# Kernel tuning notes

Hardware: AMD Instinct MI355X
Metric: run time of the kernel (lower is better)

Reference implementation:

```python
import jax, jax.numpy as jnp
import numpy as np

B, D = 65536, 1024
E = 10   # experts per group (shared and per-task)
H = 10   # expert hidden units
T = 2    # tasks
G = 20   # gate units = task experts + shared experts


def setup_inputs() -> dict:
    key = jax.random.key(0)
    ks = jax.random.split(key, 8)
    s = 1.0 / np.sqrt(D)
    return {
        "x": jax.random.normal(ks[0], (B, D), dtype=jnp.float32),
        "show_index": jax.random.randint(ks[1], (B,), 0, 100, dtype=jnp.int64),
        "st": jax.random.normal(ks[2], (B, 8), dtype=jnp.float32),
        "Ws": jax.random.normal(ks[3], (E, D, H), dtype=jnp.float32) * s,
        "bs": jnp.zeros((E, H), dtype=jnp.float32),
        "Wt": jax.random.normal(ks[4], (T, E, D, H), dtype=jnp.float32) * s,
        "bt": jnp.zeros((T, E, H), dtype=jnp.float32),
        "Wg": jax.random.normal(ks[5], (T, D, G), dtype=jnp.float32) * s,
        "bg": jnp.zeros((T, G), dtype=jnp.float32),
        "Wc": jax.random.normal(ks[6], (H, 1), dtype=jnp.float32),
        "bc": jnp.zeros((1,), dtype=jnp.float32),
        "Wv": jax.random.normal(ks[7], (H, 1), dtype=jnp.float32),
        "bv": jnp.zeros((1,), dtype=jnp.float32),
    }


def reference(x, show_index, st, Ws, bs, Wt, bt, Wg, bg, Wc, bc, Wv, bv):
    # shared experts: [B, H, E]  (Dense(H,relu) per expert, stacked on axis 2)
    share = jax.nn.relu(jnp.einsum('bd,edh->bhe', x, Ws) + bs.T)

    def task_tower(i):
        gate = jax.nn.softmax(x @ Wg[i] + bg[i], axis=-1)               # [B, G]
        task = jax.nn.relu(jnp.einsum('bd,edh->bhe', x, Wt[i]) + bt[i].T)  # [B, H, E]
        merge = jnp.concatenate([task, share], axis=2)                  # [B, H, G]
        # gate broadcast over H (repeat_elements on axis 1), sum over experts
        return jnp.sum(merge * gate[:, None, :], axis=2)                # [B, H]

    f0 = task_tower(0)
    f1 = task_tower(1)
    ctr_logits = jax.nn.sigmoid(f0 @ Wc + bc)  # [B, 1]
    cvr_logits = jax.nn.sigmoid(f1 @ Wv + bv)  # [B, 1]
    return (ctr_logits, cvr_logits)
```

## Files before the change

### kernel.cpp

```cpp
#include <hip/hip_runtime.h>
#include <hip/hip_bf16.h>

typedef __attribute__((ext_vector_type(8))) short bf16x8;
typedef __attribute__((ext_vector_type(4))) float f32x4;

#define NCOLP 384
#define STEP_SHORTS (NCOLP * 32)
#define STEP_BYTES 24576
#define SEG_BYTES 6144
#define NSTEP 32
#define HSTEP 16
#define BROWS 65536

static __device__ __forceinline__ unsigned int bf16rne(float f) {
  unsigned int u = __float_as_uint(f);
  return (u + 0x7FFFu + ((u >> 16) & 1u)) >> 16;
}
static __device__ __forceinline__ unsigned int pack2(float a, float b) {
  return bf16rne(a) | (bf16rne(b) << 16);
}

__global__ void ple_prep(const float* __restrict__ Ws, const float* __restrict__ bs,
                         const float* __restrict__ Wt, const float* __restrict__ bt,
                         const float* __restrict__ Wg, const float* __restrict__ bg,
                         unsigned short* __restrict__ Wpack, float* __restrict__ bias) {
  const int n = blockIdx.x;
  const int tid = threadIdx.x;
  const float* src = nullptr;
  int stride = 0;
  float bval = 0.f;
  if (n < 200) {
    int t = n / 100, m = n % 100, e = m / 10, h = m % 10;
    src = Wt + (size_t)(t * 10 + e) * 10240 + h;
    stride = 10;
    bval = bt[(t * 10 + e) * 10 + h];
  } else if (n < 300) {
    int m = n - 200, e = m / 10, h = m % 10;
    src = Ws + (size_t)e * 10240 + h;
    stride = 10;
    bval = bs[e * 10 + h];
  } else if (n < 340) {
    int m = n - 300, t = m / 20, g = m % 20;
    src = Wg + (size_t)t * 20480 + g;
    stride = 20;
    bval = bg[t * 20 + g];
  }
  for (int j = 0; j < 4; j++) {
    int k = tid + j * 256;
    float v = src ? src[(size_t)k * stride] : 0.f;
    Wpack[(size_t)(k >> 5) * STEP_SHORTS + ((k >> 3) & 3) * (NCOLP * 8) + n * 8 +
          (k & 7)] = (unsigned short)bf16rne(v);
  }
  if (tid == 0 && n < 352) bias[n] = bval;
}

__global__ __launch_bounds__(256, 2) void ple_main(
    const float* __restrict__ x, const unsigned short* __restrict__ Wpack,
    const float* __restrict__ bias, const float* __restrict__ Wc,
    const float* __restrict__ bc, const float* __restrict__ Wv,
    const float* __restrict__ bv, float* __restrict__ out) {
  __shared__ __align__(16) char smem[65536];
  float* z = (float*)smem;

  const int tid = threadIdx.x;
  const int l = tid & 63, w = tid >> 6;
  const int arow = l & 15, ablk = l >> 4;
  const int rowbase = blockIdx.x * 64;

  const f32x4 fzero = {0.f, 0.f, 0.f, 0.f};
  f32x4 acc[4][6];
#pragma unroll
  for (int i = 0; i < 4; ++i)
#pragma unroll
    for (int j = 0; j < 6; ++j) acc[i][j] = fzero;

  const char* bbase = (const char*)Wpack + ablk * SEG_BYTES +
                      (w * 96 + arow) * 16;
  bf16x8 bA[6], bB[6];

#pragma unroll
  for (int nt = 0; nt < 6; nt++)
    bA[nt] = *(const bf16x8*)(bbase + nt * 256);

  for (int half = 0; half < 2; ++half) {
    {
      const char* xb = (const char*)x + (size_t)(rowbase + w) * 4096 +
                       (size_t)half * 2048 + l * 32;
#pragma unroll 4
      for (int j = 0; j < 16; j++) {
        const float4 f0 = *(const float4*)(xb + (size_t)j * 4 * 4096);
        const float4 f1 = *(const float4*)(xb + (size_t)j * 4 * 4096 + 16);
        const int row = w + j * 4;
        char* dst = smem + row * 1024 + ((l ^ (row & 7)) * 16);
        *(uint4*)dst = make_uint4(pack2(f0.x, f0.y), pack2(f0.z, f0.w),
                                  pack2(f1.x, f1.y), pack2(f1.z, f1.w));
      }
    }
    __syncthreads();

#define STEP(ksl, bc_, bn_)                                                    \
  {                                                                            \
    const int kk = half * HSTEP + (ksl);                                       \
    const int kn = (kk + 1 < NSTEP) ? kk + 1 : NSTEP - 1;                      \
    const char* bp = bbase + (size_t)kn * STEP_BYTES;                          \
    _Pragma("unroll") for (int nt = 0; nt < 6; nt++)                           \
        bn_[nt] = *(const bf16x8*)(bp + nt * 256);                             \
    _Pragma("unroll") for (int mf = 0; mf < 4; mf++) {                         \
      const bf16x8 av = *(const bf16x8*)(smem + (mf * 16 + arow) * 1024 +      \
                                         ((((ksl)*4 + ablk) ^ (arow & 7)) *    \
                                          16));                                \
      _Pragma("unroll") for (int nt = 0; nt < 6; nt++)                         \
          acc[mf][nt] = __builtin_amdgcn_mfma_f32_16x16x32_bf16(               \
              av, bc_[nt], acc[mf][nt], 0, 0, 0);                              \
    }                                                                          \
  }
#pragma unroll
    for (int kp = 0; kp < 8; kp++) {
      STEP(2 * kp, bA, bB)
      STEP(2 * kp + 1, bB, bA)
    }
#undef STEP
    __syncthreads();
  }

#pragma unroll
  for (int p = 0; p < 2; p++) {
    __syncthreads();
#pragma unroll
    for (int q = 0; q < 2; q++) {
      const int mf = p * 2 + q;
#pragma unroll
      for (int nt = 0; nt < 6; nt++) {
        if (w == 3 && nt >= 4) continue;
#pragma unroll
        for (int r = 0; r < 4; r++)
          z[(q * 16 + ablk * 4 + r) * 357 + w * 96 + nt * 16 + arow] =
              acc[mf][nt][r];
      }
    }
    __syncthreads();
    if (tid < 64) {
      const int t = tid >> 5, r = tid & 31;
      const float* zr = &z[r * 357];
      float gl[20], m = -1e30f;
#pragma unroll
      for (int u = 0; u < 20; u++) {
        gl[u] = zr[300 + t * 20 + u] + bias[300 + t * 20 + u];
        m = fmaxf(m, gl[u]);
      }
      float pr[20], s = 0.f;
#pragma unroll
      for (int u = 0; u < 20; u++) {
        pr[u] = __expf(gl[u] - m);
        s += pr[u];
      }
      const float inv = 1.f / s;
      const float* Wl = t ? Wv : Wc;
      float wl[10];
#pragma unroll
      for (int h = 0; h < 10; h++) wl[h] = Wl[h];
      float accum = 0.f;
#pragma unroll
      for (int u = 0; u < 10; u++) {
        float d = 0.f;
#pragma unroll
        for (int h = 0; h < 10; h++) {
          int c = t * 100 + u * 10 + h;
          d += fmaxf(zr[c] + bias[c], 0.f) * wl[h];
        }
        accum += pr[u] * d;
      }
#pragma unroll
      for (int u = 0; u < 10; u++) {
        float d = 0.f;
#pragma unroll
        for (int h = 0; h < 10; h++) {
          int c = 200 + u * 10 + h;
          d += fmaxf(zr[c] + bias[c], 0.f) * wl[h];
        }
        accum += pr[10 + u] * d;
      }
      float logit = (t ? bv[0] : bc[0]) + accum * inv;
      out[(size_t)t * BROWS + rowbase + p * 32 + r] =
          1.f / (1.f + __expf(-logit));
    }
  }
}

extern "C" void kernel_launch(void* const* d_in, const int* in_sizes, int n_in,
                              void* d_out, int out_size, void* d_ws, size_t ws_size,
                              hipStream_t stream) {
  const float* x = (const float*)d_in[0];
  const float* Ws = (const float*)d_in[3];
  const float* bs = (const float*)d_in[4];
  const float* Wt = (const float*)d_in[5];
  const float* bt = (const float*)d_in[6];
  const float* Wg = (const float*)d_in[7];
  const float* bg = (const float*)d_in[8];
  const float* Wc = (const float*)d_in[9];
  const float* bc = (const float*)d_in[10];
  const float* Wv = (const float*)d_in[11];
  const float* bv = (const float*)d_in[12];
  unsigned short* Wpack = (unsigned short*)d_ws;
  float* bias = (float*)((char*)d_ws + (size_t)NCOLP * 1024 * 2);
  float* out = (float*)d_out;

  hipLaunchKernelGGL(ple_prep, dim3(NCOLP), dim3(256), 0, stream, Ws, bs, Wt, bt,
                     Wg, bg, Wpack, bias);
  hipLaunchKernelGGL(ple_main, dim3(BROWS / 64), dim3(256), 0, stream, x, Wpack,
                     bias, Wc, bc, Wv, bv, out);
}
```

Measured before the change: 88.56 us.

## Use 8 waves per block with 48-column slices and quarter-K LDS staging

Doubles the block to 512 threads (8 waves), so each wave computes 48 instead of 96 output columns. This halves the accumulator and B-fragment registers per thread. The x tile is staged in four 256-column quarters in a 32KB LDS buffer instead of two halves in 64KB, with a new swizzle and a load pattern that issues all loads before packing. The aim is higher occupancy and more memory parallelism for the x stream, at the cost of more barriers, more redundant B-weight loads per block, and an epilogue that runs on only 32 threads per 16-row chunk.

```diff
diff --git a/kernel.cpp b/kernel.cpp
--- a/kernel.cpp
+++ b/kernel.cpp
@@ -9,7 +9,6 @@
 #define STEP_BYTES 24576
 #define SEG_BYTES 6144
 #define NSTEP 32
-#define HSTEP 16
 #define BROWS 65536
 
 static __device__ __forceinline__ unsigned int bf16rne(float f) {
@@ -54,12 +53,12 @@
   if (tid == 0 && n < 352) bias[n] = bval;
 }
 
-__global__ __launch_bounds__(256, 2) void ple_main(
+__global__ __launch_bounds__(512, 4) void ple_main(
     const float* __restrict__ x, const unsigned short* __restrict__ Wpack,
     const float* __restrict__ bias, const float* __restrict__ Wc,
     const float* __restrict__ bc, const float* __restrict__ Wv,
     const float* __restrict__ bv, float* __restrict__ out) {
-  __shared__ __align__(16) char smem[65536];
+  __shared__ __align__(16) char smem[32768];
   float* z = (float*)smem;
 
   const int tid = threadIdx.x;
@@ -68,54 +67,63 @@
   const int rowbase = blockIdx.x * 64;
 
   const f32x4 fzero = {0.f, 0.f, 0.f, 0.f};
-  f32x4 acc[4][6];
+  f32x4 acc[4][3];
 #pragma unroll
   for (int i = 0; i < 4; ++i)
 #pragma unroll
-    for (int j = 0; j < 6; ++j) acc[i][j] = fzero;
+    for (int j = 0; j < 3; ++j) acc[i][j] = fzero;
 
   const char* bbase = (const char*)Wpack + ablk * SEG_BYTES +
-                      (w * 96 + arow) * 16;
-  bf16x8 bA[6], bB[6];
-
-#pragma unroll
-  for (int nt = 0; nt < 6; nt++)
+                      (w * 48 + arow) * 16;
+  bf16x8 bA[3], bB[3];
+
+#pragma unroll
+  for (int nt = 0; nt < 3; nt++)
     bA[nt] = *(const bf16x8*)(bbase + nt * 256);
 
-  for (int half = 0; half < 2; ++half) {
+  const int r0 = tid >> 5, s0 = tid & 31;
+  const char* xrow = (const char*)x + (size_t)(rowbase + r0) * 4096 + s0 * 32;
+
+  for (int q = 0; q < 4; ++q) {
     {
-      const char* xb = (const char*)x + (size_t)(rowbase + w) * 4096 +
-                       (size_t)half * 2048 + l * 32;
-#pragma unroll 4
-      for (int j = 0; j < 16; j++) {
-        const float4 f0 = *(const float4*)(xb + (size_t)j * 4 * 4096);
-        const float4 f1 = *(const float4*)(xb + (size_t)j * 4 * 4096 + 16);
-        const int row = w + j * 4;
-        char* dst = smem + row * 1024 + ((l ^ (row & 7)) * 16);
-        *(uint4*)dst = make_uint4(pack2(f0.x, f0.y), pack2(f0.z, f0.w),
-                                  pack2(f1.x, f1.y), pack2(f1.z, f1.w));
+      const char* sbase = xrow + q * 1024;
+      float4 f[8];
+#pragma unroll
+      for (int j = 0; j < 4; j++) {
+        f[2 * j] = *(const float4*)(sbase + (size_t)j * 16 * 4096);
+        f[2 * j + 1] = *(const float4*)(sbase + (size_t)j * 16 * 4096 + 16);
+      }
+#pragma unroll
+      for (int j = 0; j < 4; j++) {
+        const int row = r0 + j * 16;
+        const int segp = (s0 & 24) | ((s0 & 7) ^ (row & 7));
+        *(uint4*)(smem + row * 512 + segp * 16) =
+            make_uint4(pack2(f[2 * j].x, f[2 * j].y),
+                       pack2(f[2 * j].z, f[2 * j].w),
+                       pack2(f[2 * j + 1].x, f[2 * j + 1].y),
+                       pack2(f[2 * j + 1].z, f[2 * j + 1].w));
       }
     }
     __syncthreads();
 
 #define STEP(ksl, bc_, bn_)                                                    \
   {                                                                            \
-    const int kk = half * HSTEP + (ksl);                                       \
+    const int kk = q * 8 + (ksl);                                              \
     const int kn = (kk + 1 < NSTEP) ? kk + 1 : NSTEP - 1;                      \
     const char* bp = bbase + (size_t)kn * STEP_BYTES;                          \
-    _Pragma("unroll") for (int nt = 0; nt < 6; nt++)                           \
+    _Pragma("unroll") for (int nt = 0; nt < 3; nt++)                           \
         bn_[nt] = *(const bf16x8*)(bp + nt * 256);                             \
     _Pragma("unroll") for (int mf = 0; mf < 4; mf++) {                         \
-      const bf16x8 av = *(const bf16x8*)(smem + (mf * 16 + arow) * 1024 +      \
-                                         ((((ksl)*4 + ablk) ^ (arow & 7)) *    \
-                                          16));                                \
-      _Pragma("unroll") for (int nt = 0; nt < 6; nt++)                         \
+      const int segp = ((ksl)*4 & 24) | ((((ksl)&1) * 4 + ablk) ^ (arow & 7)); \
+      const bf16x8 av =                                                        \
+          *(const bf16x8*)(smem + (mf * 16 + arow) * 512 + segp * 16);         \
+      _Pragma("unroll") for (int nt = 0; nt < 3; nt++)                         \
           acc[mf][nt] = __builtin_amdgcn_mfma_f32_16x16x32_bf16(               \
               av, bc_[nt], acc[mf][nt], 0, 0, 0);                              \
     }                                                                          \
   }
 #pragma unroll
-    for (int kp = 0; kp < 8; kp++) {
+    for (int kp = 0; kp < 4; kp++) {
       STEP(2 * kp, bA, bB)
       STEP(2 * kp + 1, bB, bA)
     }
@@ -124,23 +132,18 @@
   }
 
 #pragma unroll
-  for (int p = 0; p < 2; p++) {
-    __syncthreads();
-#pragma unroll
-    for (int q = 0; q < 2; q++) {
-      const int mf = p * 2 + q;
-#pragma unroll
-      for (int nt = 0; nt < 6; nt++) {
-        if (w == 3 && nt >= 4) continue;
+  for (int p = 0; p < 4; p++) {
+#pragma unroll
+    for (int nt = 0; nt < 3; nt++) {
+      if (!(w == 7 && nt >= 1)) {
 #pragma unroll
         for (int r = 0; r < 4; r++)
-          z[(q * 16 + ablk * 4 + r) * 357 + w * 96 + nt * 16 + arow] =
-              acc[mf][nt][r];
-      }
-    }
-    __syncthreads();
-    if (tid < 64) {
-      const int t = tid >> 5, r = tid & 31;
+          z[(ablk * 4 + r) * 357 + w * 48 + nt * 16 + arow] = acc[p][nt][r];
+      }
+    }
+    __syncthreads();
+    if (tid < 32) {
+      const int t = tid >> 4, r = tid & 15;
       const float* zr = &z[r * 357];
       float gl[20], m = -1e30f;
 #pragma unroll
@@ -181,9 +184,10 @@
         accum += pr[10 + u] * d;
       }
       float logit = (t ? bv[0] : bc[0]) + accum * inv;
-      out[(size_t)t * BROWS + rowbase + p * 32 + r] =
+      out[(size_t)t * BROWS + rowbase + p * 16 + r] =
           1.f / (1.f + __expf(-logit));
     }
+    __syncthreads();
   }
 }
 
@@ -207,6 +211,6 @@
 
   hipLaunchKernelGGL(ple_prep, dim3(NCOLP), dim3(256), 0, stream, Ws, bs, Wt, bt,
                      Wg, bg, Wpack, bias);
-  hipLaunchKernelGGL(ple_main, dim3(BROWS / 64), dim3(256), 0, stream, x, Wpack,
+  hipLaunchKernelGGL(ple_main, dim3(BROWS / 64), dim3(512), 0, stream, x, Wpack,
                      bias, Wc, bc, Wv, bv, out);
 }
```

Result: slower. 122.9 us (+38.7%).
